# Optimization experiments

Hardware: AMD Instinct MI355X
Metric: run time of the kernel (lower is better)

## Reference

```python
import jax, jax.numpy as jnp
import numpy as np

N_EMBD = 384
N_HEAD = 6
HEAD_SIZE = N_EMBD // N_HEAD  # 64
BLOCK = 64
EPS = 1e-5


def _layernorm(x, g, b):
    mu = jnp.mean(x, axis=-1, keepdims=True)
    var = jnp.mean(jnp.square(x - mu), axis=-1, keepdims=True)
    return (x - mu) * jax.lax.rsqrt(var + EPS) * g + b


def setup_inputs() -> dict:
    key = jax.random.key(0)
    ks = jax.random.split(key, 12)
    s = 0.02
    return {
        "x": jax.random.normal(ks[0], (1024, BLOCK, N_EMBD), dtype=jnp.float32),
        "ln1_g": jnp.ones((N_EMBD,), jnp.float32),
        "ln1_b": jnp.zeros((N_EMBD,), jnp.float32),
        "Wq": jax.random.normal(ks[1], (N_HEAD, N_EMBD, HEAD_SIZE), jnp.float32) * s,
        "Wk": jax.random.normal(ks[2], (N_HEAD, N_EMBD, HEAD_SIZE), jnp.float32) * s,
        "Wv": jax.random.normal(ks[3], (N_HEAD, N_EMBD, HEAD_SIZE), jnp.float32) * s,
        "Wo": jax.random.normal(ks[4], (N_EMBD, N_EMBD), jnp.float32) * s,
        "bo": jnp.zeros((N_EMBD,), jnp.float32),
        "ln2_g": jnp.ones((N_EMBD,), jnp.float32),
        "ln2_b": jnp.zeros((N_EMBD,), jnp.float32),
        "W1": jax.random.normal(ks[5], (N_EMBD, 4 * N_EMBD), jnp.float32) * s,
        "b1": jnp.zeros((4 * N_EMBD,), jnp.float32),
        "W2": jax.random.normal(ks[6], (4 * N_EMBD, N_EMBD), jnp.float32) * s,
        "b2": jnp.zeros((N_EMBD,), jnp.float32),
    }


def reference(x, ln1_g, ln1_b, Wq, Wk, Wv, Wo, bo, ln2_g, ln2_b, W1, b1, W2, b2):
    B, T, C = x.shape
    # --- multi-head causal self-attention on ln1(x) ---
    xn = _layernorm(x, ln1_g, ln1_b)
    q = jnp.einsum('btc,hcd->bhtd', xn, Wq)
    k = jnp.einsum('btc,hcd->bhtd', xn, Wk)
    v = jnp.einsum('btc,hcd->bhtd', xn, Wv)
    scale = HEAD_SIZE ** -0.5
    att = jnp.einsum('bhtd,bhsd->bhts', q, k) * scale
    causal = jnp.tril(jnp.ones((T, T), bool))
    att = jnp.where(causal, att, -jnp.inf)
    att = jax.nn.softmax(att, axis=-1)  # dropout is identity at eval
    out = jnp.einsum('bhts,bhsd->bhtd', att, v)
    out = out.transpose(0, 2, 1, 3).reshape(B, T, C)  # concat heads
    x = x + out @ Wo + bo
    # --- feed-forward on ln2(x) ---
    xn2 = _layernorm(x, ln2_g, ln2_b)
    h = jax.nn.relu(xn2 @ W1 + b1)
    x = x + h @ W2 + b2
    return x
```

## Files before the change

kernel.cpp:

```cpp
#include <hip/hip_runtime.h>

#define TT 64
#define CC 384
#define NH 6
#define HID 1536
#define LDX 392
#define LDH 72

typedef __bf16 bf16x8 __attribute__((ext_vector_type(8)));
typedef float f32x4 __attribute__((ext_vector_type(4)));
typedef unsigned short us8 __attribute__((ext_vector_type(8)));

#define MFMA(a, b, c) __builtin_amdgcn_mfma_f32_16x16x32_bf16(a, b, c, 0, 0, 0)

static __device__ __forceinline__ unsigned short f2bf(float f) {
  unsigned u = __builtin_bit_cast(unsigned, f);
  u += 0x7FFFu + ((u >> 16) & 1u);
  return (unsigned short)(u >> 16);
}
static __device__ __forceinline__ float bf2f(unsigned short h) {
  unsigned u = ((unsigned)h) << 16;
  return __builtin_bit_cast(float, u);
}
static __device__ __forceinline__ bf16x8 ld8(const unsigned short* p) {
  return __builtin_bit_cast(bf16x8, *reinterpret_cast<const us8*>(p));
}

__global__ void prep_w(const float* __restrict__ Wq, const float* __restrict__ Wk,
                       const float* __restrict__ Wv, const float* __restrict__ Wo,
                       const float* __restrict__ W1, const float* __restrict__ W2,
                       unsigned short* __restrict__ ws) {
  const int T0 = 1152 * 384;
  const int T1 = T0 + 384 * 384;
  const int T2 = T1 + 1536 * 384;
  const int T3 = T2 + 384 * 1536;
  for (int i = blockIdx.x * blockDim.x + threadIdx.x; i < T3; i += gridDim.x * blockDim.x) {
    float v;
    if (i < T0) {
      int n = i / 384, k = i % 384;
      int hh = n / 192, j = n % 192;
      const float* W = (j < 64) ? Wq : (j < 128) ? Wk : Wv;
      int d = (j < 64) ? j : (j < 128) ? j - 64 : j - 128;
      v = W[((size_t)hh * 384 + k) * 64 + d];
    } else if (i < T1) {
      int i2 = i - T0; int n = i2 / 384, k = i2 % 384;
      v = Wo[(size_t)k * 384 + n];
    } else if (i < T2) {
      int i2 = i - T1; int n = i2 / 384, k = i2 % 384;
      v = W1[(size_t)k * 1536 + n];
    } else {
      int i2 = i - T2; int n = i2 / 1536, k = i2 % 1536;
      v = W2[(size_t)k * 384 + n];
    }
    ws[i] = f2bf(v);
  }
}

__global__ __launch_bounds__(256, 2)
void attn_fwd(const float* __restrict__ x,
              const float* __restrict__ ln1g, const float* __restrict__ ln1b,
              const float* __restrict__ bo,
              const unsigned short* __restrict__ Wqkv,
              const unsigned short* __restrict__ WoT,
              float* __restrict__ x2) {
  __shared__ unsigned short sXN[TT * LDX];
  __shared__ unsigned short sHEAD[3 * TT * LDH];
  unsigned short* sQ = sHEAD;
  unsigned short* sK = sHEAD + TT * LDH;
  unsigned short* sV = sHEAD + 2 * TT * LDH;

  const int b = blockIdx.x;
  const int tid = threadIdx.x;
  const int wv = tid >> 6;
  const int ln = tid & 63;
  const int l16 = ln & 15;
  const int lg = ln >> 4;
  const float* xb = x + (size_t)b * TT * CC;
  const f32x4 Z4 = {0.f, 0.f, 0.f, 0.f};

#pragma unroll 1
  for (int r = wv * 16; r < wv * 16 + 16; ++r) {
    float v[6], s = 0.f, sq = 0.f;
#pragma unroll
    for (int j = 0; j < 6; ++j) { v[j] = xb[r * CC + ln + 64 * j]; s += v[j]; sq += v[j] * v[j]; }
#pragma unroll
    for (int off = 32; off; off >>= 1) { s += __shfl_xor(s, off); sq += __shfl_xor(sq, off); }
    float mu = s * (1.f / CC);
    float rs = rsqrtf(sq * (1.f / CC) - mu * mu + 1e-5f);
#pragma unroll
    for (int j = 0; j < 6; ++j) {
      int c = ln + 64 * j;
      sXN[r * LDX + c] = f2bf((v[j] - mu) * rs * ln1g[c] + ln1b[c]);
    }
  }
  __syncthreads();

  f32x4 pacc[4][6];
#pragma unroll
  for (int m = 0; m < 4; ++m)
#pragma unroll
    for (int c = 0; c < 6; ++c) pacc[m][c] = Z4;

  const unsigned short* prow[6];
#pragma unroll
  for (int c = 0; c < 6; ++c)
    prow[c] = WoT + (size_t)(wv * 96 + c * 16 + l16) * CC + 8 * lg;

#pragma unroll 1
  for (int h = 0; h < NH; ++h) {
    const unsigned short* wrow[3];
#pragma unroll
    for (int c = 0; c < 3; ++c)
      wrow[c] = Wqkv + (size_t)(h * 192 + wv * 48 + c * 16 + l16) * CC + 8 * lg;

    f32x4 qacc[4][3];
#pragma unroll
    for (int m = 0; m < 4; ++m)
#pragma unroll
      for (int c = 0; c < 3; ++c) qacc[m][c] = Z4;

    bf16x8 bpre[2][3];
#pragma unroll
    for (int c = 0; c < 3; ++c) bpre[0][c] = ld8(wrow[c] + 0);
#pragma unroll
    for (int c = 0; c < 3; ++c) bpre[1][c] = ld8(wrow[c] + 32);
#pragma unroll
    for (int kk = 0; kk < CC; kk += 32) {
      const int slot = (kk >> 5) & 1;
      bf16x8 bcur[3];
#pragma unroll
      for (int c = 0; c < 3; ++c) bcur[c] = bpre[slot][c];
      if (kk + 64 < CC) {
#pragma unroll
        for (int c = 0; c < 3; ++c) bpre[slot][c] = ld8(wrow[c] + kk + 64);
      }
      bf16x8 a[4];
#pragma unroll
      for (int m = 0; m < 4; ++m)
        a[m] = ld8(&sXN[(m * 16 + l16) * LDX + kk + 8 * lg]);
      __builtin_amdgcn_s_setprio(1);
#pragma unroll
      for (int c = 0; c < 3; ++c)
#pragma unroll
        for (int m = 0; m < 4; ++m) qacc[m][c] = MFMA(a[m], bcur[c], qacc[m][c]);
      __builtin_amdgcn_s_setprio(0);
    }
    __syncthreads();
#pragma unroll
    for (int m = 0; m < 4; ++m)
#pragma unroll
      for (int c = 0; c < 3; ++c) {
        int n = wv * 48 + c * 16 + l16;
#pragma unroll
        for (int rg = 0; rg < 4; ++rg) {
          int t = m * 16 + lg * 4 + rg;
          unsigned short bv = f2bf(qacc[m][c][rg]);
          if (n < 64) sQ[t * LDH + n] = bv;
          else if (n < 128) sK[t * LDH + (n - 64)] = bv;
          else sV[(n - 128) * LDH + t] = bv;
        }
      }
    __syncthreads();

    f32x4 sacc[4];
#pragma unroll
    for (int c = 0; c < 4; ++c) sacc[c] = Z4;
#pragma unroll
    for (int kk = 0; kk < 64; kk += 32) {
      bf16x8 a = ld8(&sQ[(wv * 16 + l16) * LDH + kk + 8 * lg]);
#pragma unroll
      for (int c = 0; c < 4; ++c) {
        bf16x8 bb = ld8(&sK[(c * 16 + l16) * LDH + kk + 8 * lg]);
        sacc[c] = MFMA(a, bb, sacc[c]);
      }
    }
#pragma unroll
    for (int rg = 0; rg < 4; ++rg) {
      int row = wv * 16 + lg * 4 + rg;
      float e[4], mx = -1e30f;
#pragma unroll
      for (int c = 0; c < 4; ++c) {
        int col = c * 16 + l16;
        float vv = sacc[c][rg] * 0.125f;
        e[c] = (col <= row) ? vv : -1e30f;
        mx = fmaxf(mx, e[c]);
      }
#pragma unroll
      for (int off = 8; off; off >>= 1) mx = fmaxf(mx, __shfl_xor(mx, off));
      float sum = 0.f;
#pragma unroll
      for (int c = 0; c < 4; ++c) {
        int col = c * 16 + l16;
        e[c] = (col <= row) ? __expf(e[c] - mx) : 0.f;
        sum += e[c];
      }
#pragma unroll
      for (int off = 8; off; off >>= 1) sum += __shfl_xor(sum, off);
      float inv = 1.f / sum;
#pragma unroll
      for (int c = 0; c < 4; ++c)
        sQ[row * LDH + c * 16 + l16] = f2bf(e[c] * inv);
    }

    bf16x8 pb[2][6];
#pragma unroll
    for (int s2 = 0; s2 < 2; ++s2)
#pragma unroll
      for (int c = 0; c < 6; ++c)
        pb[s2][c] = ld8(prow[c] + h * 64 + 32 * s2);

    f32x4 oacc[4];
#pragma unroll
    for (int c = 0; c < 4; ++c) oacc[c] = Z4;
#pragma unroll
    for (int kk = 0; kk < 64; kk += 32) {
      bf16x8 a = ld8(&sQ[(wv * 16 + l16) * LDH + kk + 8 * lg]);
#pragma unroll
      for (int c = 0; c < 4; ++c) {
        bf16x8 bb = ld8(&sV[(c * 16 + l16) * LDH + kk + 8 * lg]);
        oacc[c] = MFMA(a, bb, oacc[c]);
      }
    }
    __syncthreads();
#pragma unroll
    for (int c = 0; c < 4; ++c)
#pragma unroll
      for (int rg = 0; rg < 4; ++rg) {
        int t = wv * 16 + lg * 4 + rg;
        sK[t * LDH + c * 16 + l16] = f2bf(oacc[c][rg]);
      }
    __syncthreads();

    __builtin_amdgcn_s_setprio(1);
#pragma unroll
    for (int kk = 0; kk < 64; kk += 32) {
      const int slot = kk >> 5;
      bf16x8 a[4];
#pragma unroll
      for (int m = 0; m < 4; ++m)
        a[m] = ld8(&sK[(m * 16 + l16) * LDH + kk + 8 * lg]);
#pragma unroll
      for (int c = 0; c < 6; ++c)
#pragma unroll
        for (int m = 0; m < 4; ++m) pacc[m][c] = MFMA(a[m], pb[slot][c], pacc[m][c]);
    }
    __builtin_amdgcn_s_setprio(0);
  }

  float* xo = x2 + (size_t)b * TT * CC;
#pragma unroll
  for (int m = 0; m < 4; ++m)
#pragma unroll
    for (int c = 0; c < 6; ++c) {
      int n = wv * 96 + c * 16 + l16;
      float bov = bo[n];
#pragma unroll
      for (int rg = 0; rg < 4; ++rg) {
        int t = m * 16 + lg * 4 + rg;
        xo[t * CC + n] = xb[t * CC + n] + pacc[m][c][rg] + bov;
      }
    }
}

__global__ __launch_bounds__(512, 4)
void mlp_fwd(const float* __restrict__ ln2g, const float* __restrict__ ln2b,
             const float* __restrict__ b1, const float* __restrict__ b2,
             const unsigned short* __restrict__ W1T,
             const unsigned short* __restrict__ W2T,
             float* xo) {
  __shared__ unsigned short sXN[24576];
  __shared__ unsigned short sH[8192];

  const int b = blockIdx.x;
  const int tid = threadIdx.x;
  const int wv = tid >> 6;
  const int ln = tid & 63;
  const int l16 = ln & 15;
  const int lg = ln >> 4;
  float* xb = xo + (size_t)b * TT * CC;
  const f32x4 Z4 = {0.f, 0.f, 0.f, 0.f};
  const int rx = (l16 ^ lg) << 3;

#pragma unroll 1
  for (int r = wv * 8; r < wv * 8 + 8; ++r) {
    float v[6], s = 0.f, sq = 0.f;
#pragma unroll
    for (int j = 0; j < 6; ++j) { v[j] = xb[r * CC + ln + 64 * j]; s += v[j]; sq += v[j] * v[j]; }
#pragma unroll
    for (int off = 32; off; off >>= 1) { s += __shfl_xor(s, off); sq += __shfl_xor(sq, off); }
    float mu = s * (1.f / CC);
    float rs = rsqrtf(sq * (1.f / CC) - mu * mu + 1e-5f);
    int m = r >> 4, row16 = r & 15;
#pragma unroll
    for (int j = 0; j < 6; ++j) {
      int c = ln + 64 * j;
      int sl = c >> 5, ks = (c >> 3) & 3, off = c & 7;
      sXN[(((m * 12 + sl) * 4 + ks) * 16 + (row16 ^ ks)) * 8 + off] =
          f2bf((v[j] - mu) * rs * ln2g[c] + ln2b[c]);
    }
  }
  __syncthreads();

  f32x4 macc[4][3];
#pragma unroll
  for (int m = 0; m < 4; ++m)
#pragma unroll
    for (int c = 0; c < 3; ++c) macc[m][c] = Z4;

#pragma unroll 1
  for (int ch = 0; ch < 12; ++ch) {
    f32x4 hacc[4];
#pragma unroll
    for (int m = 0; m < 4; ++m) hacc[m] = Z4;

    const unsigned short* w1p = W1T + (size_t)(ch * 128 + wv * 16 + l16) * CC + 8 * lg;
    bf16x8 bpre[2];
    bpre[0] = ld8(w1p);
    bpre[1] = ld8(w1p + 32);
#pragma unroll
    for (int sl = 0; sl < 12; ++sl) {
      const int slot = sl & 1;
      bf16x8 bcur = bpre[slot];
      if (sl + 2 < 12) bpre[slot] = ld8(w1p + (sl + 2) * 32);
      bf16x8 a[4];
#pragma unroll
      for (int m = 0; m < 4; ++m)
        a[m] = ld8(&sXN[((m * 48 + sl * 4 + lg) << 7) + rx]);
      __builtin_amdgcn_s_setprio(1);
#pragma unroll
      for (int m = 0; m < 4; ++m) hacc[m] = MFMA(a[m], bcur, hacc[m]);
      __builtin_amdgcn_s_setprio(0);
    }

    float b1v = b1[ch * 128 + wv * 16 + l16];
    const unsigned short* w2p = W2T + (size_t)(wv * 48 + l16) * HID + ch * 128 + 8 * lg;
    bf16x8 c2[3];
#pragma unroll
    for (int c = 0; c < 3; ++c) c2[c] = ld8(w2p + (size_t)(c * 16) * HID);

    __syncthreads();

    {
      int nl = wv * 16 + l16;
      int slh = nl >> 5, ks = (nl >> 3) & 3, off = nl & 7;
#pragma unroll
      for (int m = 0; m < 4; ++m)
#pragma unroll
        for (int rg = 0; rg < 4; ++rg) {
          int row16 = lg * 4 + rg;
          sH[(((m * 4 + slh) * 4 + ks) * 16 + (row16 ^ ks)) * 8 + off] =
              f2bf(fmaxf(hacc[m][rg] + b1v, 0.f));
        }
    }
    __syncthreads();

#pragma unroll
    for (int sl = 0; sl < 4; ++sl) {
      bf16x8 a2[4];
#pragma unroll
      for (int m = 0; m < 4; ++m)
        a2[m] = ld8(&sH[((m * 16 + sl * 4 + lg) << 7) + rx]);
      bf16x8 nxt[3];
      if (sl < 3) {
#pragma unroll
        for (int c = 0; c < 3; ++c) nxt[c] = ld8(w2p + (size_t)(c * 16) * HID + (sl + 1) * 32);
      }
      __builtin_amdgcn_s_setprio(1);
#pragma unroll
      for (int c = 0; c < 3; ++c)
#pragma unroll
        for (int m = 0; m < 4; ++m) macc[m][c] = MFMA(a2[m], c2[c], macc[m][c]);
      __builtin_amdgcn_s_setprio(0);
      if (sl < 3) {
#pragma unroll
        for (int c = 0; c < 3; ++c) c2[c] = nxt[c];
      }
    }
  }

#pragma unroll
  for (int m = 0; m < 4; ++m)
#pragma unroll
    for (int c = 0; c < 3; ++c) {
      int n = wv * 48 + c * 16 + l16;
      float b2v = b2[n];
#pragma unroll
      for (int rg = 0; rg < 4; ++rg) {
        int t = m * 16 + lg * 4 + rg;
        size_t idx = (size_t)t * CC + n;
        float x2v = xb[idx];
        xb[idx] = x2v + macc[m][c][rg] + b2v;
      }
    }
}

extern "C" void kernel_launch(void* const* d_in, const int* in_sizes, int n_in,
                              void* d_out, int out_size, void* d_ws, size_t ws_size,
                              hipStream_t stream) {
  const float* x    = (const float*)d_in[0];
  const float* ln1g = (const float*)d_in[1];
  const float* ln1b = (const float*)d_in[2];
  const float* Wq   = (const float*)d_in[3];
  const float* Wk   = (const float*)d_in[4];
  const float* Wv   = (const float*)d_in[5];
  const float* Wo   = (const float*)d_in[6];
  const float* bo   = (const float*)d_in[7];
  const float* ln2g = (const float*)d_in[8];
  const float* ln2b = (const float*)d_in[9];
  const float* W1   = (const float*)d_in[10];
  const float* b1   = (const float*)d_in[11];
  const float* W2   = (const float*)d_in[12];
  const float* b2   = (const float*)d_in[13];
  unsigned short* ws = (unsigned short*)d_ws;

  const size_t need = (size_t)(1152 * 384 + 384 * 384 + 1536 * 384 + 384 * 1536) * 2;
  if (ws_size < need) return;

  hipLaunchKernelGGL(prep_w, dim3(1024), dim3(256), 0, stream, Wq, Wk, Wv, Wo, W1, W2, ws);

  const unsigned short* Wqkv = ws;
  const unsigned short* WoT  = ws + 1152 * 384;
  const unsigned short* W1T  = WoT + 384 * 384;
  const unsigned short* W2T  = W1T + 1536 * 384;
  int nblk = in_sizes[0] / (TT * CC);

  hipLaunchKernelGGL(attn_fwd, dim3(nblk), dim3(256), 0, stream,
                     x, ln1g, ln1b, bo, Wqkv, WoT, (float*)d_out);
  hipLaunchKernelGGL(mlp_fwd, dim3(nblk), dim3(512), 0, stream,
                     ln2g, ln2b, b1, b2, W1T, W2T, (float*)d_out);
}
```

Measured before the change: 484.9 us.

## Split MLP kernel into 32-row blocks of 256 threads with wider per-wave tiles

The MLP kernel now handles 32 tokens per block with 4 waves instead of 64 tokens with 8 waves, and launches twice as many blocks. Each wave computes two 16-wide hidden column tiles and six output column tiles over two row tiles, and the shared-memory buffers shrink to match. The software prefetch of W2 fragments across k-slices is removed, so those loads are issued inline. The intent is smaller blocks and less LDS per block for better occupancy and scheduling. In exchange, each weight fragment is reused across fewer rows, so W1/W2 traffic from cache doubles and W2 load latency is less hidden.

After: 730.9 us. +50.7%, slower.

```diff
diff --git a/kernel.cpp b/kernel.cpp
--- a/kernel.cpp
+++ b/kernel.cpp
@@ -262,22 +262,22 @@
     }
 }
 
-__global__ __launch_bounds__(512, 4)
+__global__ __launch_bounds__(256, 4)
 void mlp_fwd(const float* __restrict__ ln2g, const float* __restrict__ ln2b,
              const float* __restrict__ b1, const float* __restrict__ b2,
              const unsigned short* __restrict__ W1T,
              const unsigned short* __restrict__ W2T,
              float* xo) {
-  __shared__ unsigned short sXN[24576];
-  __shared__ unsigned short sH[8192];
-
-  const int b = blockIdx.x;
+  __shared__ unsigned short sXN[12288];
+  __shared__ unsigned short sH[4096];
+
+  const int bb = blockIdx.x;
   const int tid = threadIdx.x;
   const int wv = tid >> 6;
   const int ln = tid & 63;
   const int l16 = ln & 15;
   const int lg = ln >> 4;
-  float* xb = xo + (size_t)b * TT * CC;
+  float* xb = xo + (size_t)bb * 32 * CC;
   const f32x4 Z4 = {0.f, 0.f, 0.f, 0.f};
   const int rx = (l16 ^ lg) << 3;
 
@@ -301,88 +301,99 @@
   }
   __syncthreads();
 
-  f32x4 macc[4][3];
-#pragma unroll
-  for (int m = 0; m < 4; ++m)
-#pragma unroll
-    for (int c = 0; c < 3; ++c) macc[m][c] = Z4;
+  f32x4 macc[2][6];
+#pragma unroll
+  for (int m = 0; m < 2; ++m)
+#pragma unroll
+    for (int c = 0; c < 6; ++c) macc[m][c] = Z4;
+
+  const unsigned short* w2base = W2T + (size_t)(wv * 96 + l16) * HID + 8 * lg;
 
 #pragma unroll 1
   for (int ch = 0; ch < 12; ++ch) {
-    f32x4 hacc[4];
-#pragma unroll
-    for (int m = 0; m < 4; ++m) hacc[m] = Z4;
-
-    const unsigned short* w1p = W1T + (size_t)(ch * 128 + wv * 16 + l16) * CC + 8 * lg;
-    bf16x8 bpre[2];
-    bpre[0] = ld8(w1p);
-    bpre[1] = ld8(w1p + 32);
+    f32x4 hacc[2][2];
+#pragma unroll
+    for (int m = 0; m < 2; ++m)
+#pragma unroll
+      for (int c = 0; c < 2; ++c) hacc[m][c] = Z4;
+
+    const unsigned short* w1p[2];
+#pragma unroll
+    for (int c = 0; c < 2; ++c)
+      w1p[c] = W1T + (size_t)(ch * 128 + wv * 32 + c * 16 + l16) * CC + 8 * lg;
+
+    bf16x8 bpre[2][2];
+#pragma unroll
+    for (int c = 0; c < 2; ++c) bpre[0][c] = ld8(w1p[c]);
+#pragma unroll
+    for (int c = 0; c < 2; ++c) bpre[1][c] = ld8(w1p[c] + 32);
 #pragma unroll
     for (int sl = 0; sl < 12; ++sl) {
       const int slot = sl & 1;
-      bf16x8 bcur = bpre[slot];
-      if (sl + 2 < 12) bpre[slot] = ld8(w1p + (sl + 2) * 32);
-      bf16x8 a[4];
-#pragma unroll
-      for (int m = 0; m < 4; ++m)
+      bf16x8 bcur[2];
+#pragma unroll
+      for (int c = 0; c < 2; ++c) bcur[c] = bpre[slot][c];
+      if (sl + 2 < 12) {
+#pragma unroll
+        for (int c = 0; c < 2; ++c) bpre[slot][c] = ld8(w1p[c] + (sl + 2) * 32);
+      }
+      bf16x8 a[2];
+#pragma unroll
+      for (int m = 0; m < 2; ++m)
         a[m] = ld8(&sXN[((m * 48 + sl * 4 + lg) << 7) + rx]);
       __builtin_amdgcn_s_setprio(1);
 #pragma unroll
-      for (int m = 0; m < 4; ++m) hacc[m] = MFMA(a[m], bcur, hacc[m]);
+      for (int c = 0; c < 2; ++c)
+#pragma unroll
+        for (int m = 0; m < 2; ++m) hacc[m][c] = MFMA(a[m], bcur[c], hacc[m][c]);
       __builtin_amdgcn_s_setprio(0);
     }
 
-    float b1v = b1[ch * 128 + wv * 16 + l16];
-    const unsigned short* w2p = W2T + (size_t)(wv * 48 + l16) * HID + ch * 128 + 8 * lg;
-    bf16x8 c2[3];
-#pragma unroll
-    for (int c = 0; c < 3; ++c) c2[c] = ld8(w2p + (size_t)(c * 16) * HID);
-
-    __syncthreads();
-
-    {
-      int nl = wv * 16 + l16;
-      int slh = nl >> 5, ks = (nl >> 3) & 3, off = nl & 7;
-#pragma unroll
-      for (int m = 0; m < 4; ++m)
+    float b1c[2];
+#pragma unroll
+    for (int c = 0; c < 2; ++c) b1c[c] = b1[ch * 128 + wv * 32 + c * 16 + l16];
+    const unsigned short* w2p = w2base + ch * 128;
+
+    __syncthreads();
+
+#pragma unroll
+    for (int m = 0; m < 2; ++m)
+#pragma unroll
+      for (int c = 0; c < 2; ++c) {
+        int nl = wv * 32 + c * 16 + l16;
+        int slh = nl >> 5, ks = (nl >> 3) & 3, off = nl & 7;
 #pragma unroll
         for (int rg = 0; rg < 4; ++rg) {
           int row16 = lg * 4 + rg;
           sH[(((m * 4 + slh) * 4 + ks) * 16 + (row16 ^ ks)) * 8 + off] =
-              f2bf(fmaxf(hacc[m][rg] + b1v, 0.f));
+              f2bf(fmaxf(hacc[m][c][rg] + b1c[c], 0.f));
         }
-    }
+      }
     __syncthreads();
 
 #pragma unroll
     for (int sl = 0; sl < 4; ++sl) {
-      bf16x8 a2[4];
-#pragma unroll
-      for (int m = 0; m < 4; ++m)
+      bf16x8 c2[6];
+#pragma unroll
+      for (int c = 0; c < 6; ++c) c2[c] = ld8(w2p + (size_t)(c * 16) * HID + sl * 32);
+      bf16x8 a2[2];
+#pragma unroll
+      for (int m = 0; m < 2; ++m)
         a2[m] = ld8(&sH[((m * 16 + sl * 4 + lg) << 7) + rx]);
-      bf16x8 nxt[3];
-      if (sl < 3) {
-#pragma unroll
-        for (int c = 0; c < 3; ++c) nxt[c] = ld8(w2p + (size_t)(c * 16) * HID + (sl + 1) * 32);
-      }
       __builtin_amdgcn_s_setprio(1);
 #pragma unroll
-      for (int c = 0; c < 3; ++c)
-#pragma unroll
-        for (int m = 0; m < 4; ++m) macc[m][c] = MFMA(a2[m], c2[c], macc[m][c]);
+      for (int c = 0; c < 6; ++c)
+#pragma unroll
+        for (int m = 0; m < 2; ++m) macc[m][c] = MFMA(a2[m], c2[c], macc[m][c]);
       __builtin_amdgcn_s_setprio(0);
-      if (sl < 3) {
-#pragma unroll
-        for (int c = 0; c < 3; ++c) c2[c] = nxt[c];
-      }
     }
   }
 
 #pragma unroll
-  for (int m = 0; m < 4; ++m)
-#pragma unroll
-    for (int c = 0; c < 3; ++c) {
-      int n = wv * 48 + c * 16 + l16;
+  for (int m = 0; m < 2; ++m)
+#pragma unroll
+    for (int c = 0; c < 6; ++c) {
+      int n = wv * 96 + c * 16 + l16;
       float b2v = b2[n];
 #pragma unroll
       for (int rg = 0; rg < 4; ++rg) {
@@ -426,6 +437,6 @@
 
   hipLaunchKernelGGL(attn_fwd, dim3(nblk), dim3(256), 0, stream,
                      x, ln1g, ln1b, bo, Wqkv, WoT, (float*)d_out);
-  hipLaunchKernelGGL(mlp_fwd, dim3(nblk), dim3(512), 0, stream,
+  hipLaunchKernelGGL(mlp_fwd, dim3(nblk * 2), dim3(256), 0, stream,
                      ln2g, ln2b, b1, b2, W1T, W2T, (float*)d_out);
 }
```
